# Kernel tuning notes

Hardware: AMD Instinct MI355X
Metric: run time of the kernel (lower is better)

The kernel has to match this reference:

```python
import jax, jax.numpy as jnp
import numpy as np

THRESHOLD = 0.5  # default threshold from MemoryPool.update

N, D, P, C0 = 16384, 1024, 4096, 2048


def setup_inputs() -> dict:
    key = jax.random.key(0)
    k1, k2, k3, k4 = jax.random.split(key, 4)
    summaries = jax.random.normal(k1, (N, D), dtype=jnp.float32)
    scores = jax.random.uniform(k2, (N,), dtype=jnp.float32)
    slot = jnp.arange(P)
    # slots >= count are empty (zeros), matching fresh torch buffers
    pool = jnp.where((slot < C0)[:, None],
                     jax.random.normal(k3, (P, D), dtype=jnp.float32), 0.0)
    priorities = jnp.where(slot < C0,
                           jax.random.uniform(k4, (P,), dtype=jnp.float32), 0.0)
    return {"summaries": summaries, "scores": scores,
            "pool": pool, "priorities": priorities, "count": C0}


def reference(summaries, scores, pool, priorities, count):
    pool_size = pool.shape[0]
    cnt0 = jnp.asarray(count, jnp.int32)

    def step(carry, xc):
        pl, pr, cnt = carry
        s, sc = xc  # (D,), ()
        valid = sc > THRESHOLD
        min_idx = jnp.argmin(pr)
        has_room = cnt < pool_size
        idx = jnp.where(has_room, cnt, min_idx)
        replace_ok = sc > pr[min_idx]
        do_write = valid & (has_room | replace_ok)
        new_pl = jnp.where(do_write, pl.at[idx].set(s), pl)
        new_pr = jnp.where(do_write, pr.at[idx].set(sc), pr)
        new_cnt = cnt + (do_write & has_room).astype(jnp.int32)
        return (new_pl, new_pr, new_cnt), None

    (pool_out, prior_out, cnt_out), _ = jax.lax.scan(
        step, (pool, priorities, cnt0), (summaries, scores))
    return pool_out, prior_out, cnt_out
```

## Files before the change

kernel.cpp:

```cpp
#include <hip/hip_runtime.h>

typedef unsigned long long u64;
#define THRESH 0.5f
#define ALL1 0xFFFFFFFFFFFFFFFFull
#define FINF __builtin_inff()

__device__ __forceinline__ u64 shflxU64(u64 v, int m) { return __shfl_xor(v, m, 64); }
__device__ __forceinline__ void sort64(u64 &key, int lane) {
#pragma unroll
    for (int k = 2; k <= 64; k <<= 1) {
#pragma unroll
        for (int j = k >> 1; j > 0; j >>= 1) {
            u64 p = shflxU64(key, j);
            bool takeMax = ((lane & j) != 0) != ((lane & k) != 0);
            u64 mn = key < p ? key : p;
            u64 mx = key < p ? p : key;
            key = takeMax ? mx : mn;
        }
    }
}

__device__ __forceinline__ u64 mkey(float v, int id) {
    v = (v == 0.0f) ? 0.0f : v;
    unsigned u = __float_as_uint(v);
    u ^= (unsigned)((int)u >> 31) | 0x80000000u;
    return ((u64)u << 32) | (unsigned)id;
}

__global__ __launch_bounds__(1024) void k1_scan(
    const float* __restrict__ scores, const float* __restrict__ priorities,
    const int* __restrict__ countPtr, int N, int P,
    float* __restrict__ outPrior, float* __restrict__ outCnt, int* __restrict__ srcWs,
    float* __restrict__ cval, int* __restrict__ csrc, int* __restrict__ meta)
{
    const int tid = threadIdx.x;
    for (int s = tid; s < P; s += 1024) { outPrior[s] = priorities[s]; srcWs[s] = -1; }
    int C0 = *countPtr; C0 = C0 < 0 ? 0 : (C0 > P ? P : C0);
    const int per = (N + 1023) >> 10;
    const int i0 = tid * per;
    float sv[16];
    if (per == 16 && i0 + 16 <= N) {
        const float4* s4 = (const float4*)(scores + i0);
        const float4 a = s4[0], b = s4[1], c4 = s4[2], d = s4[3];
        sv[0]=a.x; sv[1]=a.y; sv[2]=a.z; sv[3]=a.w;
        sv[4]=b.x; sv[5]=b.y; sv[6]=b.z; sv[7]=b.w;
        sv[8]=c4.x; sv[9]=c4.y; sv[10]=c4.z; sv[11]=c4.w;
        sv[12]=d.x; sv[13]=d.y; sv[14]=d.z; sv[15]=d.w;
    } else {
#pragma unroll 16
        for (int j = 0; j < 16; ++j)
            sv[j] = (j < per && i0 + j < N) ? scores[i0 + j] : 0.f;
    }
    int c = 0;
#pragma unroll 16
    for (int j = 0; j < 16; ++j) c += (j < per && i0 + j < N && sv[j] > THRESH) ? 1 : 0;
    __shared__ int sb[1024];
    sb[tid] = c; __syncthreads();
    for (int off = 1; off < 1024; off <<= 1) {
        int v = (tid >= off) ? sb[tid - off] : 0;
        __syncthreads();
        sb[tid] += v;
        __syncthreads();
    }
    const int total = sb[1023];
    int v = sb[tid] - c;
    int A = P - C0; if (A > total) A = total; if (A < 0) A = 0;
#pragma unroll 16
    for (int j = 0; j < 16; ++j) {
        if (j < per && i0 + j < N) {
            const float sc = sv[j];
            if (sc > THRESH) {
                if (v < A) { outPrior[C0 + v] = sc; srcWs[C0 + v] = i0 + j; }
                else { cval[v - A] = sc; csrc[v - A] = i0 + j; }
                ++v;
            }
        }
    }
    if (tid == 0) {
        meta[0] = total - A;
        meta[1] = C0 + A;
        outCnt[0] = (float)(C0 + A);
    }
}

#define K2T 512
__global__ __launch_bounds__(256) void k2_count(
    const float* __restrict__ outPrior, const float* __restrict__ cval,
    const int* __restrict__ meta, int* __restrict__ cnt2)
{
    const int M = meta[0], F = meta[1];
    const int iB = blockIdx.x << 8;
    if (iB >= M) return;
    const int hi = min(M, iB + 256);
    const int smax = F + hi;
    const int tb = blockIdx.y * K2T;
    if (tb >= smax) return;
    const int te = min(smax - tb, K2T);
    __shared__ __align__(16) float tile[K2T];
    for (int t = threadIdx.x; t < K2T; t += 256) {
        const int s = tb + t;
        tile[t] = (t < te) ? ((s < F) ? outPrior[s] : cval[s - F]) : FINF;
    }
    __syncthreads();
    const int i = iB + threadIdx.x;
    if (i >= M) return;
    const float x = cval[i];
    int cnt = 0;
    const float4* t4 = (const float4*)tile;
    if (tb + K2T <= F + iB) {
#pragma unroll 8
        for (int q = 0; q < K2T / 4; ++q) {
            const float4 w = t4[q];
            cnt += (w.x < x) + (w.y < x) + (w.z < x) + (w.w < x);
        }
    } else {
        int lim = F + i - tb;
        if (lim < 0) lim = 0;
        if (lim > te) lim = te;
        const int l4 = lim >> 2;
        for (int q = 0; q < l4; ++q) {
            const float4 w = t4[q];
            cnt += (w.x < x) + (w.y < x) + (w.z < x) + (w.w < x);
        }
        for (int t = l4 << 2; t < lim; ++t) cnt += tile[t] < x;
    }
    if (cnt) atomicAdd(&cnt2[i], cnt);
}

__global__ __launch_bounds__(1024) void k3_compact(
    const float* __restrict__ cval, const int* __restrict__ csrc,
    const int* __restrict__ cnt2, int* __restrict__ meta,
    float* __restrict__ cvalS, float* __restrict__ wval, int* __restrict__ wsrc,
    int* __restrict__ writeNum)
{
    const int M = meta[0];
    const int tid = threadIdx.x;
    const int per = (M + 1023) >> 10;
    const int i0 = tid * per, i1 = min(i0 + per, M);
    int c = 0;
    for (int i = i0; i < i1; ++i) c += (cnt2[i] >= i + 1) ? 1 : 0;
    __shared__ int sb[1024];
    sb[tid] = c; __syncthreads();
    for (int off = 1; off < 1024; off <<= 1) {
        int v = (tid >= off) ? sb[tid - off] : 0;
        __syncthreads();
        sb[tid] += v;
        __syncthreads();
    }
    int w = sb[tid] - c;
    for (int i = i0; i < i1; ++i) {
        if (cnt2[i] >= i + 1) {
            wval[w] = cval[i]; wsrc[w] = csrc[i]; writeNum[i] = w; cvalS[i] = cval[i]; ++w;
        } else { writeNum[i] = -1; cvalS[i] = FINF; }
    }
    if (tid == 0) meta[2] = sb[1023];
}

#define K4T 512
__global__ __launch_bounds__(256) void k4_count(
    const float* __restrict__ outPrior, const float* __restrict__ cvalS,
    const int* __restrict__ meta, int P, int* __restrict__ cnt4)
{
    const int M = meta[0], F = meta[1];
    if (M == 0) return;
    const int tot = F + M;
    const int eB = blockIdx.x << 8;
    if (eB >= tot) return;
    const int tb = blockIdx.y * K4T;
    if (tb >= tot) return;
    const int te = min(tot - tb, K4T);
    __shared__ __align__(16) u64 tile[K4T];
    for (int t = threadIdx.x; t < K4T; t += 256) {
        const int s = tb + t;
        u64 kk = ALL1;
        if (t < te) {
            if (s < F) kk = mkey(outPrior[s], s);
            else       kk = mkey(cvalS[s - F], P + (s - F));
        }
        tile[t] = kk;
    }
    __syncthreads();
    const int e = eB + threadIdx.x;
    if (e >= tot) return;
    float x; int id;
    if (e < F) { x = outPrior[e]; id = e; }
    else {
        x = cvalS[e - F];
        if (x == FINF) return;
        id = P + (e - F);
    }
    const u64 kx = mkey(x, id);
    int cnt = 0;
    const ulonglong2* t2 = (const ulonglong2*)tile;
#pragma unroll 8
    for (int q = 0; q < K4T / 2; ++q) {
        const ulonglong2 w = t2[q];
        cnt += (int)(w.x < kx) + (int)(w.y < kx);
    }
    if (cnt) atomicAdd(&cnt4[e], cnt);
}

__global__ __launch_bounds__(256) void k4_scatter(
    const float* __restrict__ outPrior, const float* __restrict__ cvalS,
    const int* __restrict__ writeNum, const int* __restrict__ meta, int P,
    const int* __restrict__ cnt4,
    float* __restrict__ evV, int* __restrict__ evId, int* __restrict__ survW)
{
    const int M = meta[0], F = meta[1], R = meta[2];
    if (M == 0) return;
    const int tot = F + M;
    const int e = blockIdx.x * 256 + threadIdx.x;
    if (e >= tot) return;
    float x; int myid; bool isCand = false; int wn = -1;
    if (e < F) { x = outPrior[e]; myid = e; }
    else {
        const int i = e - F;
        x = cvalS[i];
        if (x == FINF) return;
        isCand = true; wn = writeNum[i]; myid = P + i;
    }
    const int cnt = cnt4[e];
    if (isCand) survW[wn] = (cnt >= R) ? 1 : 0;
    if (cnt < R + 64) { evV[cnt] = x; evId[cnt] = isCand ? (P + wn) : myid; }
}

#define SCAP 14400
#define MSF   (1 << 29)
#define DONEF (1 << 30)
#define SLOTM ((1 << 29) - 1)
__global__ __launch_bounds__(1024) void k5_chain(
    const float* __restrict__ evV, const int* __restrict__ evId,
    const int* __restrict__ meta, int P,
    int* __restrict__ Sg, int* __restrict__ survW)
{
    __shared__ int state[SCAP];
    __shared__ int shRp, shLeft;
    const int tid = threadIdx.x;
    const int R = meta[2];
    if (R <= 0 || R > SCAP) return;
    const int F = meta[1];
    const int Wtot = F + R;

    if (tid == 0) {
        int Rp = R;
        if (R < Wtot) {
            const float vR1 = evV[R - 1];
            if (evV[R] == vR1) {
                int rr = R - 1;
                while (rr >= 0 && evV[rr] == vR1) --rr;
                Rp = rr + 1;
            }
        }
        shRp = Rp;
    }
    __syncthreads();
    const int Rp = shRp;

    for (int r = tid; r < Rp; r += 1024) state[r] = 0;
    __syncthreads();

    for (int round = 0; round < Rp + 2; ++round) {
        for (int r = tid; r < Rp; r += 1024) {
            if (state[r] & (DONEF | MSF)) continue;
            int cur = r, ms = -1;
            while (true) {
                const int id = evId[cur];
                if (id < P) { ms = id; break; }
                const int p = id - P;
                if (p >= cur || p < 0) break;
                const int sp = state[p];
                if (sp & DONEF) { ms = sp & SLOTM; break; }
                const float v = evV[p];
                const bool tiedP = (p > 0 && evV[p - 1] == v) ||
                                   (p + 1 < Rp && evV[p + 1] == v);
                if (tiedP) break;
                cur = p;
            }
            if (ms >= 0) {
                const float v = evV[r];
                const bool tiedR = (r > 0 && evV[r - 1] == v) ||
                                   (r + 1 < Rp && evV[r + 1] == v);
                state[r] = ms | (tiedR ? MSF : (MSF | DONEF));
            }
        }
        __syncthreads();
        for (int r = tid; r < Rp; r += 1024) {
            const float v = evV[r];
            if (r > 0 && evV[r - 1] == v) continue;
            if (r + 1 >= Rp || evV[r + 1] != v) continue;
            if (state[r] & DONEF) continue;
            int re = r + 1;
            while (re < Rp && evV[re] == v) ++re;
            bool ready = true;
            for (int s = r; s < re; ++s) ready &= (state[s] & MSF) != 0;
            if (!ready) continue;
            for (int j = r; j < re; ++j) {
                int best = j;
                for (int s = j + 1; s < re; ++s)
                    if ((state[s] & SLOTM) < (state[best] & SLOTM)) best = s;
                const int tmp = state[best];
                state[best] = state[j];
                state[j] = tmp;
            }
            for (int j = r; j < re; ++j) state[j] |= DONEF;
        }
        __syncthreads();
        if (tid == 0) shLeft = 0;
        __syncthreads();
        int loc = 0;
        for (int r = tid; r < Rp; r += 1024) loc += (state[r] & DONEF) ? 0 : 1;
        if (loc) atomicAdd(&shLeft, loc);
        __syncthreads();
        if (shLeft == 0) break;
    }

    for (int r = tid; r < Rp; r += 1024) Sg[r] = state[r] & SLOTM;
    __syncthreads();

    if (Rp < R && tid < 64) {
        const int lane = tid;
        const int r = Rp + lane;
        const float v0 = evV[Rp];
        const bool mem = (r < Wtot) && (evV[r] == v0);
        const int g = (int)__popcll(__ballot(mem));
        const int e = R - Rp;
        int id = 0, ms = 0;
        if (mem) {
            id = evId[r];
            ms = (id < P) ? id : (state[id - P] & SLOTM);
        }
        u64 key = mem ? ((((u64)(unsigned)ms) << 32) | (u64)(unsigned)id) : ALL1;
        sort64(key, lane);
        const int sid = (int)(unsigned)(key & 0xFFFFFFFFull);
        const int sms = (int)(unsigned)(key >> 32);
        const bool real = (key != ALL1) && (lane < g);
        if (real && lane < e) Sg[Rp + lane] = sms;
        if (real && sid >= P) survW[sid - P] = (lane >= e) ? 1 : 0;
    }
}

__global__ __launch_bounds__(256) void k5b_apply(
    const int* __restrict__ Sg, const int* __restrict__ survW,
    const float* __restrict__ wval, const int* __restrict__ wsrc,
    const int* __restrict__ meta,
    float* __restrict__ outPrior, int* __restrict__ srcWs)
{
    const int R = meta[2];
    const int j = blockIdx.x * 256 + threadIdx.x;
    if (j >= R) return;
    if (survW[j]) {
        const int s = Sg[j];
        outPrior[s] = wval[j];
        srcWs[s] = wsrc[j];
    }
}

__global__ __launch_bounds__(256) void gather_kernel(
    const float* __restrict__ summaries,
    const float* __restrict__ pool,
    const int* __restrict__ src,
    float* __restrict__ outPool, int D) {
    int p = blockIdx.x;
    int s = src[p];
    const float* row = (s >= 0) ? (summaries + (size_t)s * D) : (pool + (size_t)p * D);
    float* o = outPool + (size_t)p * D;
    if ((D & 3) == 0) {
        for (int k = (threadIdx.x << 2); k < D; k += (blockDim.x << 2)) {
            float4 v = *(const float4*)(row + k);
            *(float4*)(o + k) = v;
        }
    } else {
        for (int k = threadIdx.x; k < D; k += blockDim.x) o[k] = row[k];
    }
}

extern "C" void kernel_launch(void* const* d_in, const int* in_sizes, int n_in,
                              void* d_out, int out_size, void* d_ws, size_t ws_size,
                              hipStream_t stream) {
    const float* summaries  = (const float*)d_in[0];
    const float* scores     = (const float*)d_in[1];
    const float* pool       = (const float*)d_in[2];
    const float* priorities = (const float*)d_in[3];
    const int*   count      = (const int*)d_in[4];

    int N = in_sizes[1];
    int P = in_sizes[3];
    int D = in_sizes[0] / N;

    float* outPool  = (float*)d_out;
    float* outPrior = outPool + (size_t)P * D;
    float* outCnt   = outPrior + P;
    int*   srcWs    = (int*)d_ws;

    float* cval     = outPool;
    int*   csrc     = (int*)outPool + 1 * N;
    float* cvalS    = outPool + 3 * N;
    float* wval     = outPool + 4 * N;
    int*   wsrc     = (int*)outPool + 5 * N;
    int*   writeNum = (int*)outPool + 6 * N;
    float* evV      = outPool + 7 * N;
    int*   evId     = (int*)outPool + 8 * N + 64;
    int*   Sgbuf    = (int*)outPool + 9 * N + 128;
    int*   survW    = (int*)outPool + 10 * N + 128;
    int*   meta     = (int*)outPool + 11 * N + 128;
    int*   cnt2     = (int*)outPool + 11 * N + 192;
    int*   cnt4     = (int*)outPool + 12 * N + 192;

    const int nb2 = (N + 255) / 256;
    const int nb4 = (P + N + 255) / 256;
    const int ty  = (P + N + K2T - 1) / K2T;

    dim3 g2(nb2, ty), g4(nb4, ty);

    hipMemsetAsync(cnt2, 0, (size_t)N * sizeof(int), stream);
    hipMemsetAsync(cnt4, 0, (size_t)(P + N) * sizeof(int), stream);

    k1_scan<<<1, 1024, 0, stream>>>(scores, priorities, count, N, P,
                                    outPrior, outCnt, srcWs, cval, csrc, meta);
    k2_count<<<g2, 256, 0, stream>>>(outPrior, cval, meta, cnt2);
    k3_compact<<<1, 1024, 0, stream>>>(cval, csrc, cnt2, meta, cvalS, wval, wsrc, writeNum);
    k4_count<<<g4, 256, 0, stream>>>(outPrior, cvalS, meta, P, cnt4);
    k4_scatter<<<nb4, 256, 0, stream>>>(outPrior, cvalS, writeNum, meta, P, cnt4,
                                        evV, evId, survW);
    k5_chain<<<1, 1024, 0, stream>>>(evV, evId, meta, P, Sgbuf, survW);
    k5b_apply<<<nb2, 256, 0, stream>>>(Sgbuf, survW, wval, wsrc, meta, outPrior, srcWs);
    gather_kernel<<<P, 256, 0, stream>>>(summaries, pool, srcWs, outPool, D);
}
```

Baseline: 181.7 us.

## Fuse pipeline stages via last-block tickets and drop memsets

```diff
diff --git a/kernel.cpp b/kernel.cpp
--- a/kernel.cpp
+++ b/kernel.cpp
@@ -4,6 +4,10 @@
 #define THRESH 0.5f
 #define ALL1 0xFFFFFFFFFFFFFFFFull
 #define FINF __builtin_inff()
+#define SCAP 14400
+#define MSF   (1 << 29)
+#define DONEF (1 << 30)
+#define SLOTM ((1 << 29) - 1)
 
 __device__ __forceinline__ u64 shflxU64(u64 v, int m) { return __shfl_xor(v, m, 64); }
 __device__ __forceinline__ void sort64(u64 &key, int lane) {
@@ -27,14 +31,18 @@
     return ((u64)u << 32) | (unsigned)id;
 }
 
-__global__ __launch_bounds__(1024) void k1_scan(
+__global__ __launch_bounds__(1024) void kA(
     const float* __restrict__ scores, const float* __restrict__ priorities,
     const int* __restrict__ countPtr, int N, int P,
     float* __restrict__ outPrior, float* __restrict__ outCnt, int* __restrict__ srcWs,
-    float* __restrict__ cval, int* __restrict__ csrc, int* __restrict__ meta)
+    float* __restrict__ cval, int* __restrict__ csrc, int* __restrict__ meta,
+    int* __restrict__ cnt2, int* __restrict__ cnt4, int* __restrict__ tickets)
 {
     const int tid = threadIdx.x;
     for (int s = tid; s < P; s += 1024) { outPrior[s] = priorities[s]; srcWs[s] = -1; }
+    for (int s = tid; s < N; s += 1024) cnt2[s] = 0;
+    for (int s = tid; s < P + N; s += 1024) cnt4[s] = 0;
+    if (tid == 0) { tickets[0] = 0; tickets[1] = 0; }
     int C0 = *countPtr; C0 = C0 < 0 ? 0 : (C0 > P ? P : C0);
     const int per = (N + 1023) >> 10;
     const int i0 = tid * per;
@@ -83,162 +91,168 @@
     }
 }
 
-#define K2T 512
-__global__ __launch_bounds__(256) void k2_count(
+__global__ __launch_bounds__(1024) void kB(
     const float* __restrict__ outPrior, const float* __restrict__ cval,
-    const int* __restrict__ meta, int* __restrict__ cnt2)
-{
-    const int M = meta[0], F = meta[1];
-    const int iB = blockIdx.x << 8;
-    if (iB >= M) return;
-    const int hi = min(M, iB + 256);
-    const int smax = F + hi;
-    const int tb = blockIdx.y * K2T;
-    if (tb >= smax) return;
-    const int te = min(smax - tb, K2T);
-    __shared__ __align__(16) float tile[K2T];
-    for (int t = threadIdx.x; t < K2T; t += 256) {
-        const int s = tb + t;
-        tile[t] = (t < te) ? ((s < F) ? outPrior[s] : cval[s - F]) : FINF;
-    }
-    __syncthreads();
-    const int i = iB + threadIdx.x;
-    if (i >= M) return;
-    const float x = cval[i];
-    int cnt = 0;
-    const float4* t4 = (const float4*)tile;
-    if (tb + K2T <= F + iB) {
-#pragma unroll 8
-        for (int q = 0; q < K2T / 4; ++q) {
-            const float4 w = t4[q];
-            cnt += (w.x < x) + (w.y < x) + (w.z < x) + (w.w < x);
-        }
-    } else {
-        int lim = F + i - tb;
-        if (lim < 0) lim = 0;
-        if (lim > te) lim = te;
-        const int l4 = lim >> 2;
-        for (int q = 0; q < l4; ++q) {
-            const float4 w = t4[q];
-            cnt += (w.x < x) + (w.y < x) + (w.z < x) + (w.w < x);
-        }
-        for (int t = l4 << 2; t < lim; ++t) cnt += tile[t] < x;
-    }
-    if (cnt) atomicAdd(&cnt2[i], cnt);
-}
-
-__global__ __launch_bounds__(1024) void k3_compact(
-    const float* __restrict__ cval, const int* __restrict__ csrc,
-    const int* __restrict__ cnt2, int* __restrict__ meta,
+    const int* __restrict__ csrc, int* __restrict__ meta,
+    int* __restrict__ cnt2, int* __restrict__ tickets,
     float* __restrict__ cvalS, float* __restrict__ wval, int* __restrict__ wsrc,
     int* __restrict__ writeNum)
 {
-    const int M = meta[0];
+    __shared__ __align__(16) union { float tile[512]; int sb[1024]; } sm;
+    __shared__ int shLast;
     const int tid = threadIdx.x;
+    const int M = meta[0], F = meta[1];
+
+    const int iB = (int)blockIdx.x << 10;
+    const int tb = (int)blockIdx.y << 9;
+    int te = 0;
+    if (iB < M) {
+        const int hi = min(M, iB + 1024);
+        const int smax = F + hi;
+        if (tb < smax) te = min(smax - tb, 512);
+    }
+    if (te > 0) {
+        if (tid < 512) {
+            const int s = tb + tid;
+            sm.tile[tid] = (tid < te) ? ((s < F) ? outPrior[s] : cval[s - F]) : FINF;
+        }
+        __syncthreads();
+        const int i = iB + tid;
+        if (i < M) {
+            const float x = cval[i];
+            int cnt = 0;
+            const float4* t4 = (const float4*)sm.tile;
+            if (tb + 512 <= F + iB) {
+#pragma unroll 8
+                for (int q = 0; q < 128; ++q) {
+                    const float4 w = t4[q];
+                    cnt += (w.x < x) + (w.y < x) + (w.z < x) + (w.w < x);
+                }
+            } else {
+                int lim = F + i - tb;
+                if (lim < 0) lim = 0;
+                if (lim > te) lim = te;
+                const int l4 = lim >> 2;
+                for (int q = 0; q < l4; ++q) {
+                    const float4 w = t4[q];
+                    cnt += (w.x < x) + (w.y < x) + (w.z < x) + (w.w < x);
+                }
+                for (int t = l4 << 2; t < lim; ++t) cnt += sm.tile[t] < x;
+            }
+            if (cnt) atomicAdd(&cnt2[i], cnt);
+        }
+    }
+    __syncthreads();
+    if (tid == 0)
+        shLast = (atomicAdd(&tickets[0], 1) == (int)(gridDim.x * gridDim.y) - 1);
+    __syncthreads();
+    if (!shLast) return;
+
     const int per = (M + 1023) >> 10;
     const int i0 = tid * per, i1 = min(i0 + per, M);
+    int cv[16];
     int c = 0;
-    for (int i = i0; i < i1; ++i) c += (cnt2[i] >= i + 1) ? 1 : 0;
-    __shared__ int sb[1024];
-    sb[tid] = c; __syncthreads();
+    for (int i = i0, j = 0; i < i1; ++i, ++j) {
+        const int q = atomicAdd(&cnt2[i], 0);
+        cv[j] = q;
+        c += (q >= i + 1) ? 1 : 0;
+    }
+    __syncthreads();
+    sm.sb[tid] = c; __syncthreads();
     for (int off = 1; off < 1024; off <<= 1) {
-        int v = (tid >= off) ? sb[tid - off] : 0;
-        __syncthreads();
-        sb[tid] += v;
-        __syncthreads();
-    }
-    int w = sb[tid] - c;
-    for (int i = i0; i < i1; ++i) {
-        if (cnt2[i] >= i + 1) {
+        int v = (tid >= off) ? sm.sb[tid - off] : 0;
+        __syncthreads();
+        sm.sb[tid] += v;
+        __syncthreads();
+    }
+    int w = sm.sb[tid] - c;
+    for (int i = i0, j = 0; i < i1; ++i, ++j) {
+        if (cv[j] >= i + 1) {
             wval[w] = cval[i]; wsrc[w] = csrc[i]; writeNum[i] = w; cvalS[i] = cval[i]; ++w;
         } else { writeNum[i] = -1; cvalS[i] = FINF; }
     }
-    if (tid == 0) meta[2] = sb[1023];
-}
-
-#define K4T 512
-__global__ __launch_bounds__(256) void k4_count(
-    const float* __restrict__ outPrior, const float* __restrict__ cvalS,
-    const int* __restrict__ meta, int P, int* __restrict__ cnt4)
+    if (tid == 0) meta[2] = sm.sb[1023];
+}
+
+__global__ __launch_bounds__(1024) void kC(
+    float* __restrict__ outPrior, const float* __restrict__ cvalS,
+    const int* __restrict__ writeNum, const int* __restrict__ meta, int P,
+    int* __restrict__ cnt4, int* __restrict__ tickets,
+    float* __restrict__ evV, int* __restrict__ evId, int* __restrict__ survW,
+    const float* __restrict__ wval, const int* __restrict__ wsrc,
+    int* __restrict__ srcWs)
 {
+    __shared__ __align__(16) union { u64 tile[512]; int state[SCAP]; } sm;
+    __shared__ int shLast, shRp, shLeft;
+    const int tid = threadIdx.x;
     const int M = meta[0], F = meta[1];
-    if (M == 0) return;
     const int tot = F + M;
-    const int eB = blockIdx.x << 8;
-    if (eB >= tot) return;
-    const int tb = blockIdx.y * K4T;
-    if (tb >= tot) return;
-    const int te = min(tot - tb, K4T);
-    __shared__ __align__(16) u64 tile[K4T];
-    for (int t = threadIdx.x; t < K4T; t += 256) {
-        const int s = tb + t;
-        u64 kk = ALL1;
-        if (t < te) {
-            if (s < F) kk = mkey(outPrior[s], s);
-            else       kk = mkey(cvalS[s - F], P + (s - F));
-        }
-        tile[t] = kk;
-    }
-    __syncthreads();
-    const int e = eB + threadIdx.x;
-    if (e >= tot) return;
-    float x; int id;
-    if (e < F) { x = outPrior[e]; id = e; }
-    else {
-        x = cvalS[e - F];
-        if (x == FINF) return;
-        id = P + (e - F);
-    }
-    const u64 kx = mkey(x, id);
-    int cnt = 0;
-    const ulonglong2* t2 = (const ulonglong2*)tile;
+
+    const int eB = (int)blockIdx.x << 11;
+    const int tb = (int)blockIdx.y << 9;
+    int te = 0;
+    if (M > 0 && eB < tot && tb < tot) te = min(tot - tb, 512);
+    if (te > 0) {
+        if (tid < 512) {
+            const int s = tb + tid;
+            u64 kk = ALL1;
+            if (tid < te) {
+                if (s < F) kk = mkey(outPrior[s], s);
+                else       kk = mkey(cvalS[s - F], P + (s - F));
+            }
+            sm.tile[tid] = kk;
+        }
+        __syncthreads();
+        const ulonglong2* t2 = (const ulonglong2*)sm.tile;
+#pragma unroll 2
+        for (int h = 0; h < 2; ++h) {
+            const int e = eB + (h << 10) + tid;
+            if (e < tot) {
+                float x; int id; bool live = true;
+                if (e < F) { x = outPrior[e]; id = e; }
+                else {
+                    x = cvalS[e - F];
+                    if (x == FINF) live = false;
+                    id = P + (e - F);
+                }
+                if (live) {
+                    const u64 kx = mkey(x, id);
+                    int cnt = 0;
 #pragma unroll 8
-    for (int q = 0; q < K4T / 2; ++q) {
-        const ulonglong2 w = t2[q];
-        cnt += (int)(w.x < kx) + (int)(w.y < kx);
-    }
-    if (cnt) atomicAdd(&cnt4[e], cnt);
-}
-
-__global__ __launch_bounds__(256) void k4_scatter(
-    const float* __restrict__ outPrior, const float* __restrict__ cvalS,
-    const int* __restrict__ writeNum, const int* __restrict__ meta, int P,
-    const int* __restrict__ cnt4,
-    float* __restrict__ evV, int* __restrict__ evId, int* __restrict__ survW)
-{
-    const int M = meta[0], F = meta[1], R = meta[2];
-    if (M == 0) return;
-    const int tot = F + M;
-    const int e = blockIdx.x * 256 + threadIdx.x;
-    if (e >= tot) return;
-    float x; int myid; bool isCand = false; int wn = -1;
-    if (e < F) { x = outPrior[e]; myid = e; }
-    else {
-        const int i = e - F;
-        x = cvalS[i];
-        if (x == FINF) return;
-        isCand = true; wn = writeNum[i]; myid = P + i;
-    }
-    const int cnt = cnt4[e];
-    if (isCand) survW[wn] = (cnt >= R) ? 1 : 0;
-    if (cnt < R + 64) { evV[cnt] = x; evId[cnt] = isCand ? (P + wn) : myid; }
-}
-
-#define SCAP 14400
-#define MSF   (1 << 29)
-#define DONEF (1 << 30)
-#define SLOTM ((1 << 29) - 1)
-__global__ __launch_bounds__(1024) void k5_chain(
-    const float* __restrict__ evV, const int* __restrict__ evId,
-    const int* __restrict__ meta, int P,
-    int* __restrict__ Sg, int* __restrict__ survW)
-{
-    __shared__ int state[SCAP];
-    __shared__ int shRp, shLeft;
-    const int tid = threadIdx.x;
+                    for (int q = 0; q < 256; ++q) {
+                        const ulonglong2 w2 = t2[q];
+                        cnt += (int)(w2.x < kx) + (int)(w2.y < kx);
+                    }
+                    if (cnt) atomicAdd(&cnt4[e], cnt);
+                }
+            }
+        }
+    }
+    __syncthreads();
+    if (tid == 0)
+        shLast = (atomicAdd(&tickets[1], 1) == (int)(gridDim.x * gridDim.y) - 1);
+    __syncthreads();
+    if (!shLast) return;
+
     const int R = meta[2];
+    if (M > 0) {
+        for (int e = tid; e < tot; e += 1024) {
+            float x; int myid; bool isC = false; int wn = -1;
+            if (e < F) { x = outPrior[e]; myid = e; }
+            else {
+                const int i = e - F;
+                x = cvalS[i];
+                if (x == FINF) continue;
+                isC = true; wn = writeNum[i]; myid = P + i;
+            }
+            const int cnt = atomicAdd(&cnt4[e], 0);
+            if (isC) survW[wn] = (cnt >= R) ? 1 : 0;
+            if (cnt < R + 64) { evV[cnt] = x; evId[cnt] = isC ? (P + wn) : myid; }
+        }
+    }
+    __syncthreads();
+
     if (R <= 0 || R > SCAP) return;
-    const int F = meta[1];
     const int Wtot = F + R;
 
     if (tid == 0) {
@@ -256,19 +270,19 @@
     __syncthreads();
     const int Rp = shRp;
 
-    for (int r = tid; r < Rp; r += 1024) state[r] = 0;
+    for (int r = tid; r < Rp; r += 1024) sm.state[r] = 0;
     __syncthreads();
 
     for (int round = 0; round < Rp + 2; ++round) {
         for (int r = tid; r < Rp; r += 1024) {
-            if (state[r] & (DONEF | MSF)) continue;
+            if (sm.state[r] & (DONEF | MSF)) continue;
             int cur = r, ms = -1;
             while (true) {
                 const int id = evId[cur];
                 if (id < P) { ms = id; break; }
                 const int p = id - P;
                 if (p >= cur || p < 0) break;
-                const int sp = state[p];
+                const int sp = sm.state[p];
                 if (sp & DONEF) { ms = sp & SLOTM; break; }
                 const float v = evV[p];
                 const bool tiedP = (p > 0 && evV[p - 1] == v) ||
@@ -280,7 +294,7 @@
                 const float v = evV[r];
                 const bool tiedR = (r > 0 && evV[r - 1] == v) ||
                                    (r + 1 < Rp && evV[r + 1] == v);
-                state[r] = ms | (tiedR ? MSF : (MSF | DONEF));
+                sm.state[r] = ms | (tiedR ? MSF : (MSF | DONEF));
             }
         }
         __syncthreads();
@@ -288,33 +302,31 @@
             const float v = evV[r];
             if (r > 0 && evV[r - 1] == v) continue;
             if (r + 1 >= Rp || evV[r + 1] != v) continue;
-            if (state[r] & DONEF) continue;
+            if (sm.state[r] & DONEF) continue;
             int re = r + 1;
             while (re < Rp && evV[re] == v) ++re;
             bool ready = true;
-            for (int s = r; s < re; ++s) ready &= (state[s] & MSF) != 0;
+            for (int s = r; s < re; ++s) ready &= (sm.state[s] & MSF) != 0;
             if (!ready) continue;
             for (int j = r; j < re; ++j) {
                 int best = j;
                 for (int s = j + 1; s < re; ++s)
-                    if ((state[s] & SLOTM) < (state[best] & SLOTM)) best = s;
-                const int tmp = state[best];
-                state[best] = state[j];
-                state[j] = tmp;
-            }
-            for (int j = r; j < re; ++j) state[j] |= DONEF;
+                    if ((sm.state[s] & SLOTM) < (sm.state[best] & SLOTM)) best = s;
+                const int tmp = sm.state[best];
+                sm.state[best] = sm.state[j];
+                sm.state[j] = tmp;
+            }
+            for (int j = r; j < re; ++j) sm.state[j] |= DONEF;
         }
         __syncthreads();
         if (tid == 0) shLeft = 0;
         __syncthreads();
         int loc = 0;
-        for (int r = tid; r < Rp; r += 1024) loc += (state[r] & DONEF) ? 0 : 1;
+        for (int r = tid; r < Rp; r += 1024) loc += (sm.state[r] & DONEF) ? 0 : 1;
         if (loc) atomicAdd(&shLeft, loc);
         __syncthreads();
         if (shLeft == 0) break;
     }
-
-    for (int r = tid; r < Rp; r += 1024) Sg[r] = state[r] & SLOTM;
     __syncthreads();
 
     if (Rp < R && tid < 64) {
@@ -327,31 +339,24 @@
         int id = 0, ms = 0;
         if (mem) {
             id = evId[r];
-            ms = (id < P) ? id : (state[id - P] & SLOTM);
+            ms = (id < P) ? id : (sm.state[id - P] & SLOTM);
         }
         u64 key = mem ? ((((u64)(unsigned)ms) << 32) | (u64)(unsigned)id) : ALL1;
         sort64(key, lane);
         const int sid = (int)(unsigned)(key & 0xFFFFFFFFull);
         const int sms = (int)(unsigned)(key >> 32);
         const bool real = (key != ALL1) && (lane < g);
-        if (real && lane < e) Sg[Rp + lane] = sms;
+        if (real && lane < e) sm.state[Rp + lane] = sms;
         if (real && sid >= P) survW[sid - P] = (lane >= e) ? 1 : 0;
     }
-}
-
-__global__ __launch_bounds__(256) void k5b_apply(
-    const int* __restrict__ Sg, const int* __restrict__ survW,
-    const float* __restrict__ wval, const int* __restrict__ wsrc,
-    const int* __restrict__ meta,
-    float* __restrict__ outPrior, int* __restrict__ srcWs)
-{
-    const int R = meta[2];
-    const int j = blockIdx.x * 256 + threadIdx.x;
-    if (j >= R) return;
-    if (survW[j]) {
-        const int s = Sg[j];
-        outPrior[s] = wval[j];
-        srcWs[s] = wsrc[j];
+    __syncthreads();
+
+    for (int j = tid; j < R; j += 1024) {
+        if (survW[j]) {
+            const int s = sm.state[j] & SLOTM;
+            outPrior[s] = wval[j];
+            srcWs[s] = wsrc[j];
+        }
     }
 }
 
@@ -390,39 +395,32 @@
     float* outPool  = (float*)d_out;
     float* outPrior = outPool + (size_t)P * D;
     float* outCnt   = outPrior + P;
-    int*   srcWs    = (int*)d_ws;
-
-    float* cval     = outPool;
-    int*   csrc     = (int*)outPool + 1 * N;
-    float* cvalS    = outPool + 3 * N;
-    float* wval     = outPool + 4 * N;
-    int*   wsrc     = (int*)outPool + 5 * N;
-    int*   writeNum = (int*)outPool + 6 * N;
-    float* evV      = outPool + 7 * N;
-    int*   evId     = (int*)outPool + 8 * N + 64;
-    int*   Sgbuf    = (int*)outPool + 9 * N + 128;
-    int*   survW    = (int*)outPool + 10 * N + 128;
-    int*   meta     = (int*)outPool + 11 * N + 128;
-    int*   cnt2     = (int*)outPool + 11 * N + 192;
-    int*   cnt4     = (int*)outPool + 12 * N + 192;
-
-    const int nb2 = (N + 255) / 256;
-    const int nb4 = (P + N + 255) / 256;
-    const int ty  = (P + N + K2T - 1) / K2T;
-
-    dim3 g2(nb2, ty), g4(nb4, ty);
-
-    hipMemsetAsync(cnt2, 0, (size_t)N * sizeof(int), stream);
-    hipMemsetAsync(cnt4, 0, (size_t)(P + N) * sizeof(int), stream);
-
-    k1_scan<<<1, 1024, 0, stream>>>(scores, priorities, count, N, P,
-                                    outPrior, outCnt, srcWs, cval, csrc, meta);
-    k2_count<<<g2, 256, 0, stream>>>(outPrior, cval, meta, cnt2);
-    k3_compact<<<1, 1024, 0, stream>>>(cval, csrc, cnt2, meta, cvalS, wval, wsrc, writeNum);
-    k4_count<<<g4, 256, 0, stream>>>(outPrior, cvalS, meta, P, cnt4);
-    k4_scatter<<<nb4, 256, 0, stream>>>(outPrior, cvalS, writeNum, meta, P, cnt4,
-                                        evV, evId, survW);
-    k5_chain<<<1, 1024, 0, stream>>>(evV, evId, meta, P, Sgbuf, survW);
-    k5b_apply<<<nb2, 256, 0, stream>>>(Sgbuf, survW, wval, wsrc, meta, outPrior, srcWs);
+
+    int*   ws       = (int*)d_ws;
+    int*   srcWs    = ws;
+    float* cval     = (float*)(ws + P);
+    int*   csrc     = ws + P + N;
+    float* cvalS    = (float*)(ws + P + 2 * N);
+    float* wval     = (float*)(ws + P + 3 * N);
+    int*   wsrc     = ws + P + 4 * N;
+    int*   writeNum = ws + P + 5 * N;
+    float* evV      = (float*)(ws + P + 6 * N);
+    int*   evId     = ws + P + 7 * N + 64;
+    int*   survW    = ws + P + 8 * N + 128;
+    int*   cnt2     = ws + P + 9 * N + 128;
+    int*   cnt4     = ws + P + 10 * N + 128;
+    int*   meta     = ws + 2 * P + 11 * N + 128;
+    int*   tickets  = meta + 8;
+
+    const dim3 gB((N + 1023) / 1024, (P + N + 511) / 512);
+    const dim3 gC((P + N + 2047) / 2048, (P + N + 511) / 512);
+
+    kA<<<1, 1024, 0, stream>>>(scores, priorities, count, N, P,
+                               outPrior, outCnt, srcWs, cval, csrc, meta,
+                               cnt2, cnt4, tickets);
+    kB<<<gB, 1024, 0, stream>>>(outPrior, cval, csrc, meta, cnt2, tickets,
+                                cvalS, wval, wsrc, writeNum);
+    kC<<<gC, 1024, 0, stream>>>(outPrior, cvalS, writeNum, meta, P, cnt4, tickets,
+                                evV, evId, survW, wval, wsrc, srcWs);
     gather_kernel<<<P, 256, 0, stream>>>(summaries, pool, srcWs, outPool, D);
 }
```

New measurement: 201.7 us. 11.0% more time.

## Precompute tie flags in shared state and fuse apply step into chain kernel

Applied to the files above, without the earlier changes.

```diff
diff --git a/kernel.cpp b/kernel.cpp
--- a/kernel.cpp
+++ b/kernel.cpp
@@ -225,13 +225,17 @@
 }
 
 #define SCAP 14400
+#define DONEF (1 << 30)
 #define MSF   (1 << 29)
-#define DONEF (1 << 30)
-#define SLOTM ((1 << 29) - 1)
+#define TIEF  (1 << 28)
+#define RSF   (1 << 27)
+#define PAYM  ((1 << 27) - 1)
 __global__ __launch_bounds__(1024) void k5_chain(
     const float* __restrict__ evV, const int* __restrict__ evId,
     const int* __restrict__ meta, int P,
-    int* __restrict__ Sg, int* __restrict__ survW)
+    const float* __restrict__ wval, const int* __restrict__ wsrc,
+    int* __restrict__ survW,
+    float* __restrict__ outPrior, int* __restrict__ srcWs)
 {
     __shared__ int state[SCAP];
     __shared__ int shRp, shLeft;
@@ -256,51 +260,60 @@
     __syncthreads();
     const int Rp = shRp;
 
-    for (int r = tid; r < Rp; r += 1024) state[r] = 0;
+    for (int r = tid; r < Rp; r += 1024) {
+        const float v = evV[r];
+        const bool tp = (r > 0) && (evV[r - 1] == v);
+        const bool tn = (r + 1 < Rp) && (evV[r + 1] == v);
+        const bool tie = tp || tn;
+        const int rs = (tie && !tp) ? RSF : 0;
+        const int id = evId[r];
+        int st;
+        if (id < P) st = id | MSF | (tie ? (TIEF | rs) : DONEF);
+        else        st = (id - P) | (tie ? (TIEF | rs) : 0);
+        state[r] = st;
+    }
     __syncthreads();
 
     for (int round = 0; round < Rp + 2; ++round) {
         for (int r = tid; r < Rp; r += 1024) {
-            if (state[r] & (DONEF | MSF)) continue;
-            int cur = r, ms = -1;
-            while (true) {
-                const int id = evId[cur];
-                if (id < P) { ms = id; break; }
-                const int p = id - P;
-                if (p >= cur || p < 0) break;
+            const int s = state[r];
+            if (s & MSF) continue;
+            int p = s & PAYM;
+            int ms = -1;
+            for (int g = 0; g < Rp + 2; ++g) {
                 const int sp = state[p];
-                if (sp & DONEF) { ms = sp & SLOTM; break; }
-                const float v = evV[p];
-                const bool tiedP = (p > 0 && evV[p - 1] == v) ||
-                                   (p + 1 < Rp && evV[p + 1] == v);
-                if (tiedP) break;
-                cur = p;
+                if (sp & DONEF) { ms = sp & PAYM; break; }
+                if (sp & (MSF | TIEF)) break;
+                const int q = sp & PAYM;
+                if (q >= p) break;
+                p = q;
             }
-            if (ms >= 0) {
-                const float v = evV[r];
-                const bool tiedR = (r > 0 && evV[r - 1] == v) ||
-                                   (r + 1 < Rp && evV[r + 1] == v);
-                state[r] = ms | (tiedR ? MSF : (MSF | DONEF));
+            if (ms >= 0)
+                state[r] = ms | MSF | ((s & TIEF) ? (s & (TIEF | RSF)) : DONEF);
+            else
+                state[r] = p | (s & (TIEF | RSF));
+        }
+        __syncthreads();
+        for (int r = tid; r < Rp; r += 1024) {
+            const int s = state[r];
+            if (!(s & RSF) || (s & DONEF)) continue;
+            int re = r + 1;
+            while (re < Rp) {
+                const int t = state[re];
+                if ((t & TIEF) && !(t & RSF)) ++re; else break;
             }
-        }
-        __syncthreads();
-        for (int r = tid; r < Rp; r += 1024) {
-            const float v = evV[r];
-            if (r > 0 && evV[r - 1] == v) continue;
-            if (r + 1 >= Rp || evV[r + 1] != v) continue;
-            if (state[r] & DONEF) continue;
-            int re = r + 1;
-            while (re < Rp && evV[re] == v) ++re;
             bool ready = true;
-            for (int s = r; s < re; ++s) ready &= (state[s] & MSF) != 0;
+            for (int q = r; q < re; ++q) ready &= (state[q] & MSF) != 0;
             if (!ready) continue;
             for (int j = r; j < re; ++j) {
                 int best = j;
-                for (int s = j + 1; s < re; ++s)
-                    if ((state[s] & SLOTM) < (state[best] & SLOTM)) best = s;
-                const int tmp = state[best];
-                state[best] = state[j];
-                state[j] = tmp;
+                for (int q = j + 1; q < re; ++q)
+                    if ((state[q] & PAYM) < (state[best] & PAYM)) best = q;
+                if (best != j) {
+                    const int pj = state[j] & PAYM, pb = state[best] & PAYM;
+                    state[j]    = (state[j] & ~PAYM) | pb;
+                    state[best] = (state[best] & ~PAYM) | pj;
+                }
             }
             for (int j = r; j < re; ++j) state[j] |= DONEF;
         }
@@ -313,8 +326,6 @@
         __syncthreads();
         if (shLeft == 0) break;
     }
-
-    for (int r = tid; r < Rp; r += 1024) Sg[r] = state[r] & SLOTM;
     __syncthreads();
 
     if (Rp < R && tid < 64) {
@@ -327,31 +338,24 @@
         int id = 0, ms = 0;
         if (mem) {
             id = evId[r];
-            ms = (id < P) ? id : (state[id - P] & SLOTM);
+            ms = (id < P) ? id : (state[id - P] & PAYM);
         }
         u64 key = mem ? ((((u64)(unsigned)ms) << 32) | (u64)(unsigned)id) : ALL1;
         sort64(key, lane);
         const int sid = (int)(unsigned)(key & 0xFFFFFFFFull);
         const int sms = (int)(unsigned)(key >> 32);
         const bool real = (key != ALL1) && (lane < g);
-        if (real && lane < e) Sg[Rp + lane] = sms;
+        if (real && lane < e) state[Rp + lane] = sms;
         if (real && sid >= P) survW[sid - P] = (lane >= e) ? 1 : 0;
     }
-}
-
-__global__ __launch_bounds__(256) void k5b_apply(
-    const int* __restrict__ Sg, const int* __restrict__ survW,
-    const float* __restrict__ wval, const int* __restrict__ wsrc,
-    const int* __restrict__ meta,
-    float* __restrict__ outPrior, int* __restrict__ srcWs)
-{
-    const int R = meta[2];
-    const int j = blockIdx.x * 256 + threadIdx.x;
-    if (j >= R) return;
-    if (survW[j]) {
-        const int s = Sg[j];
-        outPrior[s] = wval[j];
-        srcWs[s] = wsrc[j];
+    __syncthreads();
+
+    for (int j = tid; j < R; j += 1024) {
+        if (survW[j]) {
+            const int sl = state[j] & PAYM;
+            outPrior[sl] = wval[j];
+            srcWs[sl] = wsrc[j];
+        }
     }
 }
 
@@ -400,11 +404,10 @@
     int*   writeNum = (int*)outPool + 6 * N;
     float* evV      = outPool + 7 * N;
     int*   evId     = (int*)outPool + 8 * N + 64;
-    int*   Sgbuf    = (int*)outPool + 9 * N + 128;
     int*   survW    = (int*)outPool + 10 * N + 128;
-    int*   meta     = (int*)outPool + 11 * N + 128;
     int*   cnt2     = (int*)outPool + 11 * N + 192;
     int*   cnt4     = (int*)outPool + 12 * N + 192;
+    int*   meta     = (int*)outPool + 11 * N + 128;
 
     const int nb2 = (N + 255) / 256;
     const int nb4 = (P + N + 255) / 256;
@@ -422,7 +425,7 @@
     k4_count<<<g4, 256, 0, stream>>>(outPrior, cvalS, meta, P, cnt4);
     k4_scatter<<<nb4, 256, 0, stream>>>(outPrior, cvalS, writeNum, meta, P, cnt4,
                                         evV, evId, survW);
-    k5_chain<<<1, 1024, 0, stream>>>(evV, evId, meta, P, Sgbuf, survW);
-    k5b_apply<<<nb2, 256, 0, stream>>>(Sgbuf, survW, wval, wsrc, meta, outPrior, srcWs);
+    k5_chain<<<1, 1024, 0, stream>>>(evV, evId, meta, P, wval, wsrc, survW,
+                                     outPrior, srcWs);
     gather_kernel<<<P, 256, 0, stream>>>(summaries, pool, srcWs, outPool, D);
 }
```

Result: no change. 181.0 us (-0.4%).
